# Kernel tuning notes

Hardware: AMD Instinct MI355X
Metric: run time of the kernel (lower is better)

## Reference

```python
import jax, jax.numpy as jnp
import numpy as np

B, G, N = 32, 512, 512          # batch, group (POMO rollouts), problem size
EMB, H, DK = 128, 8, 16          # embedding_dim, head_num, qkv_dim (H*DK == EMB)
E, FH, K = 8, 512, 2             # num_experts, ff_hidden_dim, top-k
SQRT_EMB = 11.313708498984761    # sqrt(128), model_params['sqrt_embedding_dim']
CLIP = 10.0                      # logit_clipping


def setup_inputs() -> dict:
    key = jax.random.key(0)
    ks = jax.random.split(key, 22)
    s = 0.05
    d = {}
    d["pref"] = jax.random.uniform(ks[0], (2,), dtype=jnp.float32)
    d["graph"] = jax.random.normal(ks[1], (B, 1, EMB), dtype=jnp.float32)
    d["capacity"] = jax.random.uniform(ks[2], (B, G), dtype=jnp.float32)
    d["encoded_nodes"] = jax.random.normal(ks[3], (B, N, EMB), dtype=jnp.float32)
    d["ninf_mask"] = jnp.zeros((B, G, N), dtype=jnp.float32)
    # hyper-network MLP (note: original has NO activations between hyper_fc layers)
    d["fc1_w"] = jax.random.normal(ks[4], (256, 2)) * s
    d["fc1_b"] = jax.random.normal(ks[5], (256,)) * s
    d["fc2_w"] = jax.random.normal(ks[6], (256, 256)) * s
    d["fc2_b"] = jax.random.normal(ks[7], (256,)) * s
    d["fc3_w"] = jax.random.normal(ks[8], (8, 256)) * s
    d["fc3_b"] = jax.random.normal(ks[9], (8,)) * s
    # hyper heads producing the attention weight matrices (Linear(embd_dim=2, out), no bias)
    d["hWq"] = jax.random.normal(ks[10], ((1 + EMB) * H * DK, 2)) * 0.02
    d["hWk"] = jax.random.normal(ks[11], (EMB * H * DK, 2)) * 0.02
    d["hWv"] = jax.random.normal(ks[12], (EMB * H * DK, 2)) * 0.02
    d["hWc"] = jax.random.normal(ks[13], (EMB * H * DK, 2)) * 0.02
    # MoE combine layer: gating (token input + 8-dim pref embedding) and E expert MLPs
    d["gate_w"] = jax.random.normal(ks[14], (H * DK, E)) * s
    d["gate_pref_w"] = jax.random.normal(ks[15], (8, E)) * s
    d["e_w1"] = jax.random.normal(ks[16], (E, FH, H * DK)) * (1.0 / np.sqrt(H * DK))
    d["e_b1"] = jnp.zeros((E, FH), dtype=jnp.float32)
    d["e_w2"] = jax.random.normal(ks[17], (E, EMB, FH)) * (1.0 / np.sqrt(FH))
    d["e_b2"] = jnp.zeros((E, EMB), dtype=jnp.float32)
    d = {k2: v.astype(jnp.float32) for k2, v in d.items()}
    return d


def _heads(x):  # [B, n, H*DK] -> [B, H, n, DK]
    b, n, _ = x.shape
    return x.reshape(b, n, H, DK).transpose(0, 2, 1, 3)


def reference(pref, graph, capacity, encoded_nodes, ninf_mask,
              fc1_w, fc1_b, fc2_w, fc2_b, fc3_w, fc3_b,
              hWq, hWk, hWv, hWc,
              gate_w, gate_pref_w, e_w1, e_b1, e_w2, e_b2):
    # ---- assign(pref): hypernet generates attention weight matrices ----
    h = fc1_w @ pref + fc1_b
    h = fc2_w @ h + fc2_b
    mid = fc3_w @ h + fc3_b                      # [8] == mid_embd_pref
    Wq = (hWq @ mid[0:2]).reshape(H * DK, 1 + EMB)
    Wk = (hWk @ mid[2:4]).reshape(H * DK, EMB)
    Wv = (hWv @ mid[4:6]).reshape(H * DK, EMB)
    Wc = (hWc @ mid[6:8]).reshape(H * DK, EMB)
    # ---- set_kv ----
    k = _heads(encoded_nodes @ Wk.T)             # [B,H,N,DK]
    v = _heads(encoded_nodes @ Wv.T)
    # ---- forward ----
    inp = jnp.concatenate(
        [jnp.broadcast_to(graph, (B, G, EMB)), capacity[:, :, None]], axis=2)
    q = _heads(inp @ Wq.T)                       # [B,H,G,DK]
    score = jnp.einsum('bhgd,bhnd->bhgn', q, k) / jnp.sqrt(jnp.float32(DK))
    score = score + ninf_mask[:, None, :, :]
    attn = jax.nn.softmax(score, axis=3)
    out = jnp.einsum('bhgn,bhnd->bhgd', attn, v)
    out = out.transpose(0, 2, 1, 3).reshape(B, G, H * DK)   # [B,G,128]
    # ---- MoE combine (noisy top-k gating, deterministic at inference) ----
    logits = out @ gate_w + mid @ gate_pref_w    # [B,G,E]
    vals, idx = jax.lax.top_k(logits, K)
    gv = jax.nn.softmax(vals, axis=-1)           # softmax over selected k (T=1)
    gates = jnp.sum(jax.nn.one_hot(idx, E, dtype=out.dtype) * gv[..., None], axis=-2)
    hdn = jax.nn.relu(jnp.einsum('bgi,ehi->bgeh', out, e_w1) + e_b1)
    y = jnp.einsum('bgeh,eoh->bgeo', hdn, e_w2) + e_b2
    moe_out = jnp.einsum('bgeo,bge->bgo', y, gates)          # [B,G,EMB]
    # ---- combine + tanh-clipped masked softmax over nodes ----
    mh = moe_out @ Wc.T                           # [B,G,EMB]
    sc = jnp.einsum('bge,bne->bgn', mh, encoded_nodes) / SQRT_EMB
    probs = jax.nn.softmax(CLIP * jnp.tanh(sc) + ninf_mask, axis=2)
    return probs
```

## Files before the change

kernel.cpp:

```cpp
#include <hip/hip_runtime.h>


typedef __attribute__((ext_vector_type(8))) __bf16 bf16x8;
typedef __attribute__((ext_vector_type(4))) float f32x4;

static constexpr long OFF_MID   = 0;
static constexpr long OFF_PREFL = 8;
static constexpr long OFF_WL    = 16;
static constexpr long OFF_WKB   = 256;
static constexpr long OFF_WVB   = 8448;
static constexpr long OFF_WCB   = 16640;
static constexpr long OFF_QB    = 24832;
static constexpr long OFF_MFLAG = 28928;
static constexpr long OFF_CNT   = 33024;
static constexpr long OFF_TOK   = 33032;
static constexpr long OFF_WGT   = 164104;
static constexpr long OFF_AO    = 295176;
static constexpr long OFF_MH    = 2392328;
static constexpr long OFF_ENCB  = 3440904;

__device__ __forceinline__ unsigned f2bf(float x) {
  union { float f; unsigned u; } v; v.f = x;
  return ((v.u + 0x7FFFu + ((v.u >> 16) & 1u)) >> 16) & 0xFFFFu;
}
__device__ __forceinline__ float bflo(unsigned u) {
  union { unsigned u; float f; } v; v.u = u << 16; return v.f;
}
__device__ __forceinline__ float bfhi(unsigned u) {
  union { unsigned u; float f; } v; v.u = u & 0xFFFF0000u; return v.f;
}

__global__ __launch_bounds__(256)
void k_prep1(const float* __restrict__ pref, const float* __restrict__ fc1w,
             const float* __restrict__ fc1b, const float* __restrict__ fc2w,
             const float* __restrict__ fc2b, const float* __restrict__ fc3w,
             const float* __restrict__ fc3b, const float* __restrict__ gpw,
             const float* __restrict__ hWq, const float* __restrict__ mask,
             const float* __restrict__ ew1, const float* __restrict__ ew2,
             const float* __restrict__ enc,
             unsigned short* __restrict__ w1b, unsigned short* __restrict__ w2b,
             unsigned short* __restrict__ encb, float* __restrict__ ws) {
  const int bid = blockIdx.x;
  const int tid = threadIdx.x;
  if (bid == 0) {
    __shared__ float h1[256];
    __shared__ float h2[256];
    __shared__ float mid[8];
    const float p0 = pref[0], p1 = pref[1];
    h1[tid] = fc1w[2*tid]*p0 + fc1w[2*tid+1]*p1 + fc1b[tid];
    __syncthreads();
    float s = 0.f;
    for (int j = 0; j < 256; ++j) s = fmaf(fc2w[tid*256+j], h1[j], s);
    h2[tid] = s + fc2b[tid];
    __syncthreads();
    if (tid < 8) {
      float s2 = 0.f;
      for (int j = 0; j < 256; ++j) s2 = fmaf(fc3w[tid*256+j], h2[j], s2);
      mid[tid] = s2 + fc3b[tid];
    }
    __syncthreads();
    if (tid < 8) {
      ws[OFF_MID + tid] = mid[tid];
      float s3 = 0.f;
      for (int i = 0; i < 8; ++i) s3 = fmaf(mid[i], gpw[i*8 + tid], s3);
      ws[OFF_PREFL + tid] = s3;
      ((int*)(ws + OFF_CNT))[tid] = 0;
    }
    if (tid >= 16 && tid < 144) {
      const int o = tid - 16;
      ws[OFF_WL + o] = hWq[((long)o*129 + 128)*2]*mid[0]
                     + hWq[((long)o*129 + 128)*2 + 1]*mid[1];
    }
    return;
  }
  if (bid <= 3072) {
    const int i = (bid-1)*256 + tid;
    const float* src;
    unsigned short* dst;
    if (i < 131072)      { src = ew1 + (long)i*4;          dst = w1b + (long)i*4; }
    else if (i < 262144) { src = ew2 + (long)(i-131072)*4; dst = w2b + (long)(i-131072)*4; }
    else                 { src = enc + (long)(i-262144)*4; dst = encb + (long)(i-262144)*4; }
    const float4 v = *(const float4*)src;
    uint2 p;
    p.x = f2bf(v.x) | (f2bf(v.y) << 16);
    p.y = f2bf(v.z) | (f2bf(v.w) << 16);
    *(uint2*)dst = p;
    return;
  }
  __shared__ int fl[8];
  const int rowbase = (bid - 3073) * 8;
  const int r = tid >> 5, seg = tid & 31;
  if (tid < 8) fl[tid] = 0;
  __syncthreads();
  const float* mrow = mask + (long)(rowbase + r)*512 + seg*16;
  int nz = 0;
#pragma unroll
  for (int c = 0; c < 4; ++c) {
    const float4 v = *(const float4*)(mrow + c*4);
    nz |= (v.x != 0.f) | (v.y != 0.f) | (v.z != 0.f) | (v.w != 0.f);
  }
  if (nz) atomicOr(&fl[r], 1);
  __syncthreads();
  if (tid < 8) ((char*)(ws + OFF_MFLAG))[rowbase + tid] = (char)fl[tid];
}

__global__ __launch_bounds__(256)
void k_prep2(const float* __restrict__ graph,
             const float* __restrict__ hWq, const float* __restrict__ hWk,
             const float* __restrict__ hWv, const float* __restrict__ hWc,
             float* __restrict__ ws) {
  const int bid = blockIdx.x;
  const int tid = threadIdx.x;
  __shared__ float mid[8];
  __shared__ float g[2][128];
  if (tid < 8) mid[tid] = ws[OFF_MID + tid];
  __syncthreads();
  if (bid < 192) {
    const int i = bid*256 + tid;
    if (i < 16384) {
      ((unsigned short*)(ws + OFF_WKB))[i] =
          (unsigned short)f2bf(hWk[2*i]*mid[2] + hWk[2*i+1]*mid[3]);
    } else if (i < 32768) {
      const int j = i - 16384;
      ((unsigned short*)(ws + OFF_WVB))[j] =
          (unsigned short)f2bf(hWv[2*j]*mid[4] + hWv[2*j+1]*mid[5]);
    } else {
      const int j = i - 32768;
      ((unsigned short*)(ws + OFF_WCB))[j] =
          (unsigned short)f2bf(hWc[2*j]*mid[6] + hWc[2*j+1]*mid[7]);
    }
    return;
  }
  const int qb = bid - 192;
  const int b0 = qb*2;
  {
    const int bb = tid >> 7, ii = tid & 127;
    g[bb][ii] = graph[(b0+bb)*128 + ii];
  }
  __syncthreads();
  const float m0 = mid[0], m1 = mid[1];
  const int bb = tid >> 7, o = tid & 127;
  const float* hq = hWq + (long)o*129*2;
  float acc = 0.f;
  for (int i2 = 0; i2 < 128; ++i2) {
    const float w = hq[2*i2]*m0 + hq[2*i2+1]*m1;
    acc = fmaf(g[bb][i2], w, acc);
  }
  ws[OFF_QB + (b0+bb)*128 + o] = acc;
}

__device__ __forceinline__ bf16x8 ld_frag(const unsigned short* base, int row, int bytecol) {
  const int addr = row*256 + (bytecol ^ ((row & 7) << 4));
  return *(const bf16x8*)((const char*)base + addr);
}

__global__ __launch_bounds__(256)
void k_kv(const unsigned short* __restrict__ encb,
          const unsigned short* __restrict__ wkb,
          const unsigned short* __restrict__ wvb,
          unsigned short* __restrict__ Kb, unsigned short* __restrict__ Vtg) {
  __shared__ unsigned short Ws[128*128];
  __shared__ unsigned short Xs[64*128];
  const int tid = threadIdx.x;
  const int nbase = blockIdx.x * 64;
  const unsigned short* Wb = blockIdx.y ? wvb : wkb;
#pragma unroll
  for (int s = 0; s < 8; ++s) {
    const int id = tid + s*256;
    const int fr = id >> 4, c16 = id & 15;
    const uint4 v = *(const uint4*)(Wb + (long)fr*128 + c16*8);
    *(uint4*)((char*)Ws + fr*256 + ((c16*16) ^ ((fr & 7) << 4))) = v;
  }
#pragma unroll
  for (int s = 0; s < 4; ++s) {
    const int id = tid + s*256;
    const int r = id >> 4, c16 = id & 15;
    const uint4 v = *(const uint4*)(encb + (long)(nbase + r)*128 + c16*8);
    *(uint4*)((char*)Xs + r*256 + ((c16*16) ^ ((r & 7) << 4))) = v;
  }
  __syncthreads();
  const int w = tid >> 6, l = tid & 63, lq = l >> 4, lr = l & 15;
  f32x4 acc[2][4];
#pragma unroll
  for (int a = 0; a < 2; ++a)
#pragma unroll
    for (int m = 0; m < 4; ++m) acc[a][m] = (f32x4){0.f, 0.f, 0.f, 0.f};
#pragma unroll
  for (int ks = 0; ks < 4; ++ks) {
    const int bcol = ks*64 + lq*16;
    const bf16x8 a0 = ld_frag(Ws, (2*w  )*16 + lr, bcol);
    const bf16x8 a1 = ld_frag(Ws, (2*w+1)*16 + lr, bcol);
    const bf16x8 b0 = ld_frag(Xs, 0*16 + lr, bcol);
    const bf16x8 b1 = ld_frag(Xs, 1*16 + lr, bcol);
    const bf16x8 b2 = ld_frag(Xs, 2*16 + lr, bcol);
    const bf16x8 b3 = ld_frag(Xs, 3*16 + lr, bcol);
    acc[0][0] = __builtin_amdgcn_mfma_f32_16x16x32_bf16(a0, b0, acc[0][0], 0, 0, 0);
    acc[0][1] = __builtin_amdgcn_mfma_f32_16x16x32_bf16(a0, b1, acc[0][1], 0, 0, 0);
    acc[0][2] = __builtin_amdgcn_mfma_f32_16x16x32_bf16(a0, b2, acc[0][2], 0, 0, 0);
    acc[0][3] = __builtin_amdgcn_mfma_f32_16x16x32_bf16(a0, b3, acc[0][3], 0, 0, 0);
    acc[1][0] = __builtin_amdgcn_mfma_f32_16x16x32_bf16(a1, b0, acc[1][0], 0, 0, 0);
    acc[1][1] = __builtin_amdgcn_mfma_f32_16x16x32_bf16(a1, b1, acc[1][1], 0, 0, 0);
    acc[1][2] = __builtin_amdgcn_mfma_f32_16x16x32_bf16(a1, b2, acc[1][2], 0, 0, 0);
    acc[1][3] = __builtin_amdgcn_mfma_f32_16x16x32_bf16(a1, b3, acc[1][3], 0, 0, 0);
  }
  if (blockIdx.y == 0) {
#pragma unroll
    for (int obi = 0; obi < 2; ++obi) {
      const int o0 = (2*w + obi)*16 + lq*4;
#pragma unroll
      for (int mb = 0; mb < 4; ++mb) {
        const long n = nbase + mb*16 + lr;
        uint2 pp;
        pp.x = f2bf(acc[obi][mb][0]) | (f2bf(acc[obi][mb][1]) << 16);
        pp.y = f2bf(acc[obi][mb][2]) | (f2bf(acc[obi][mb][3]) << 16);
        *(uint2*)(Kb + n*128 + o0) = pp;
      }
    }
  } else {
    const int b = nbase >> 9;
    const int nn0 = nbase & 511;
#pragma unroll
    for (int obi = 0; obi < 2; ++obi) {
      const int o0 = (2*w + obi)*16 + lq*4;
#pragma unroll
      for (int mb = 0; mb < 4; ++mb) {
        const int nn = nn0 + mb*16 + lr;
#pragma unroll
        for (int j = 0; j < 4; ++j) {
          const int o = o0 + j;
          Vtg[(((long)b*8 + (o >> 4))*16 + (o & 15))*512 + nn] =
              (unsigned short)f2bf(acc[obi][mb][j]);
        }
      }
    }
  }
}

__global__ __launch_bounds__(256)
void k_mh(const float* __restrict__ Y0, const float* __restrict__ Y1,
          const unsigned short* __restrict__ wcb,
          unsigned short* __restrict__ mhb) {
  __shared__ unsigned short Ws[128*128];
  __shared__ unsigned short Xs[64*128];
  const int tid = threadIdx.x;
  const int nbase = blockIdx.x * 64;
#pragma unroll
  for (int s = 0; s < 8; ++s) {
    const int id = tid + s*256;
    const int fr = id >> 4, c16 = id & 15;
    const uint4 v = *(const uint4*)(wcb + (long)fr*128 + c16*8);
    *(uint4*)((char*)Ws + fr*256 + ((c16*16) ^ ((fr & 7) << 4))) = v;
  }
#pragma unroll
  for (int s = 0; s < 4; ++s) {
    const int id = tid + s*256;
    const int r = id >> 4, c16 = id & 15;
    const long base = (long)(nbase + r)*128 + c16*8;
    const float4 a0 = *(const float4*)(Y0 + base);
    const float4 a1 = *(const float4*)(Y0 + base + 4);
    const float4 b0 = *(const float4*)(Y1 + base);
    const float4 b1 = *(const float4*)(Y1 + base + 4);
    uint4 p;
    p.x = f2bf(a0.x + b0.x) | (f2bf(a0.y + b0.y) << 16);
    p.y = f2bf(a0.z + b0.z) | (f2bf(a0.w + b0.w) << 16);
    p.z = f2bf(a1.x + b1.x) | (f2bf(a1.y + b1.y) << 16);
    p.w = f2bf(a1.z + b1.z) | (f2bf(a1.w + b1.w) << 16);
    *(uint4*)((char*)Xs + r*256 + ((c16*16) ^ ((r & 7) << 4))) = p;
  }
  __syncthreads();
  const int w = tid >> 6, l = tid & 63, lq = l >> 4, lr = l & 15;
  f32x4 acc[2][4];
#pragma unroll
  for (int a = 0; a < 2; ++a)
#pragma unroll
    for (int m = 0; m < 4; ++m) acc[a][m] = (f32x4){0.f, 0.f, 0.f, 0.f};
#pragma unroll
  for (int ks = 0; ks < 4; ++ks) {
    const int bcol = ks*64 + lq*16;
    const bf16x8 a0 = ld_frag(Ws, (2*w  )*16 + lr, bcol);
    const bf16x8 a1 = ld_frag(Ws, (2*w+1)*16 + lr, bcol);
    const bf16x8 b0 = ld_frag(Xs, 0*16 + lr, bcol);
    const bf16x8 b1 = ld_frag(Xs, 1*16 + lr, bcol);
    const bf16x8 b2 = ld_frag(Xs, 2*16 + lr, bcol);
    const bf16x8 b3 = ld_frag(Xs, 3*16 + lr, bcol);
    acc[0][0] = __builtin_amdgcn_mfma_f32_16x16x32_bf16(a0, b0, acc[0][0], 0, 0, 0);
    acc[0][1] = __builtin_amdgcn_mfma_f32_16x16x32_bf16(a0, b1, acc[0][1], 0, 0, 0);
    acc[0][2] = __builtin_amdgcn_mfma_f32_16x16x32_bf16(a0, b2, acc[0][2], 0, 0, 0);
    acc[0][3] = __builtin_amdgcn_mfma_f32_16x16x32_bf16(a0, b3, acc[0][3], 0, 0, 0);
    acc[1][0] = __builtin_amdgcn_mfma_f32_16x16x32_bf16(a1, b0, acc[1][0], 0, 0, 0);
    acc[1][1] = __builtin_amdgcn_mfma_f32_16x16x32_bf16(a1, b1, acc[1][1], 0, 0, 0);
    acc[1][2] = __builtin_amdgcn_mfma_f32_16x16x32_bf16(a1, b2, acc[1][2], 0, 0, 0);
    acc[1][3] = __builtin_amdgcn_mfma_f32_16x16x32_bf16(a1, b3, acc[1][3], 0, 0, 0);
  }
#pragma unroll
  for (int obi = 0; obi < 2; ++obi) {
    const int o0 = (2*w + obi)*16 + lq*4;
#pragma unroll
    for (int mb = 0; mb < 4; ++mb) {
      const long n = nbase + mb*16 + lr;
      uint2 pp;
      pp.x = f2bf(acc[obi][mb][0]) | (f2bf(acc[obi][mb][1]) << 16);
      pp.y = f2bf(acc[obi][mb][2]) | (f2bf(acc[obi][mb][3]) << 16);
      *(uint2*)(mhb + n*128 + o0) = pp;
    }
  }
}

__global__ __launch_bounds__(512, 8)
void k_attn(const unsigned short* __restrict__ Kb,
            const unsigned short* __restrict__ Vtg,
            const float* __restrict__ ws, const float* __restrict__ cap,
            const float* __restrict__ mask, unsigned short* __restrict__ AOb) {
  const int bid = blockIdx.x;
  const int b = bid & 31, h = (bid >> 5) & 7, qh = bid >> 8;
  __shared__ unsigned short Kbf[512*24];
  __shared__ unsigned short Vt[16*536];
  __shared__ unsigned short Ps[8*16*40];
  const int tid = threadIdx.x;
#pragma unroll
  for (int it = 0; it < 2; ++it) {
    const int i = tid + it*512;
    const int n = i >> 1, hf = i & 1;
    const uint4 kv = *(const uint4*)(Kb + (long)(b*512 + n)*128 + h*16 + hf*8);
    *(uint4*)(Kbf + n*24 + hf*8) = kv;
    const int d = i >> 6, c = i & 63;
    const uint4 vv = *(const uint4*)(Vtg + ((long)(b*8 + h)*16 + d)*512 + c*8);
    *(uint4*)(Vt + d*536 + c*8) = vv;
  }
  const int w = tid >> 6, l = tid & 63;
  const int lq = l >> 4, lr = l & 15;
  const int grow = qh*128 + w*16 + lr;
  bf16x8 qf;
  {
    union { uint4 u; bf16x8 v; } cv;
    cv.u = make_uint4(0u, 0u, 0u, 0u);
    if (lq < 2) {
      const float* qbp = ws + OFF_QB + b*128 + h*16 + lq*8;
      const float* wlp = ws + OFF_WL + h*16 + lq*8;
      const float cp = cap[b*512 + grow];
      float qv[8];
#pragma unroll
      for (int j = 0; j < 8; ++j) qv[j] = (qbp[j] + cp*wlp[j]) * 0.25f;
      cv.u.x = f2bf(qv[0]) | (f2bf(qv[1]) << 16);
      cv.u.y = f2bf(qv[2]) | (f2bf(qv[3]) << 16);
      cv.u.z = f2bf(qv[4]) | (f2bf(qv[5]) << 16);
      cv.u.w = f2bf(qv[6]) | (f2bf(qv[7]) << 16);
    }
    qf = cv.v;
  }
  const int mf = ((const char*)(ws + OFF_MFLAG))[b*512 + grow];
  const bool usemask = __any(mf != 0);
  unsigned short* Pw = Ps + w*16*40;
  const int psw = (lr & 3) << 3;
  __syncthreads();
  float lsum = 0.f;
  f32x4 oacc = {0.f, 0.f, 0.f, 0.f};
  const float* mrow = mask + ((long)(b*512 + grow))*512 + lq*4;
  for (int qc = 0; qc < 16; ++qc) {
    const int n0 = qc*32;
    f32x4 s[2];
#pragma unroll
    for (int nb = 0; nb < 2; ++nb) {
      bf16x8 kf;
      {
        union { uint4 u; bf16x8 v; } cv;
        cv.u = make_uint4(0u, 0u, 0u, 0u);
        if (lq < 2) cv.u = *(const uint4*)(Kbf + (n0 + nb*16 + lr)*24 + lq*8);
        kf = cv.v;
      }
      s[nb] = __builtin_amdgcn_mfma_f32_16x16x32_bf16(
          kf, qf, (f32x4){0.f, 0.f, 0.f, 0.f}, 0, 0, 0);
      if (usemask) {
        const float4 mk = *(const float4*)(mrow + n0 + nb*16);
        s[nb][0] += mk.x; s[nb][1] += mk.y; s[nb][2] += mk.z; s[nb][3] += mk.w;
      }
    }
#pragma unroll
    for (int nb = 0; nb < 2; ++nb) {
      const float e0 = __expf(s[nb][0]);
      const float e1 = __expf(s[nb][1]);
      const float e2 = __expf(s[nb][2]);
      const float e3 = __expf(s[nb][3]);
      lsum += (e0 + e1) + (e2 + e3);
      uint2 pp;
      asm("v_cvt_pk_bf16_f32 %0, %1, %2" : "=v"(pp.x) : "v"(e0), "v"(e1));
      asm("v_cvt_pk_bf16_f32 %0, %1, %2" : "=v"(pp.y) : "v"(e2), "v"(e3));
      *(uint2*)(Pw + lr*40 + ((nb*16 + lq*4) ^ psw)) = pp;
    }
    const bf16x8 va = *(const bf16x8*)(Vt + lr*536 + n0 + lq*8);
    const bf16x8 pb = *(const bf16x8*)(Pw + lr*40 + (lq*8 ^ psw));
    oacc = __builtin_amdgcn_mfma_f32_16x16x32_bf16(va, pb, oacc, 0, 0, 0);
  }
  lsum += __shfl_xor(lsum, 16);
  lsum += __shfl_xor(lsum, 32);
  const float inv = 1.f / lsum;
  uint2 op;
  op.x = f2bf(oacc[0]*inv) | (f2bf(oacc[1]*inv) << 16);
  op.y = f2bf(oacc[2]*inv) | (f2bf(oacc[3]*inv) << 16);
  *(uint2*)(AOb + (long)(b*512 + grow)*128 + h*16 + lq*4) = op;
}

__global__ __launch_bounds__(256)
void k_gate(const unsigned short* __restrict__ AOb, const float* __restrict__ gw,
            float* __restrict__ ws) {
  const int tid = threadIdx.x;
  const int t = blockIdx.x*256 + tid;
  const unsigned short* x = AOb + (long)t*128;
  float lg[8];
  {
    const float* pl = ws + OFF_PREFL;
#pragma unroll
    for (int e = 0; e < 8; ++e) lg[e] = pl[e];
  }
  for (int i = 0; i < 128; i += 8) {
    const uint4 xv = *(const uint4*)(x + i);
    float xf[8];
    xf[0] = bflo(xv.x); xf[1] = bfhi(xv.x);
    xf[2] = bflo(xv.y); xf[3] = bfhi(xv.y);
    xf[4] = bflo(xv.z); xf[5] = bfhi(xv.z);
    xf[6] = bflo(xv.w); xf[7] = bfhi(xv.w);
#pragma unroll
    for (int u = 0; u < 8; ++u) {
      const float xi = xf[u];
      const float4 ga = *(const float4*)(gw + (i+u)*8);
      const float4 gb = *(const float4*)(gw + (i+u)*8 + 4);
      lg[0] = fmaf(xi, ga.x, lg[0]); lg[1] = fmaf(xi, ga.y, lg[1]);
      lg[2] = fmaf(xi, ga.z, lg[2]); lg[3] = fmaf(xi, ga.w, lg[3]);
      lg[4] = fmaf(xi, gb.x, lg[4]); lg[5] = fmaf(xi, gb.y, lg[5]);
      lg[6] = fmaf(xi, gb.z, lg[6]); lg[7] = fmaf(xi, gb.w, lg[7]);
    }
  }
  int i0 = 0; float v0 = lg[0];
#pragma unroll
  for (int e = 1; e < 8; ++e) if (lg[e] > v0) { v0 = lg[e]; i0 = e; }
  int i1 = -1; float v1 = -1e30f;
#pragma unroll
  for (int e = 0; e < 8; ++e) if (e != i0 && lg[e] > v1) { v1 = lg[e]; i1 = e; }
  const float e1 = __expf(v1 - v0);
  const float w0 = 1.f / (1.f + e1);
  const float w1 = 1.f - w0;
  __shared__ int bcnt[8];
  __shared__ int gbase[8];
  if (tid < 8) bcnt[tid] = 0;
  __syncthreads();
  const int p0 = atomicAdd(&bcnt[i0], 1);
  const int p1 = atomicAdd(&bcnt[i1], 1);
  __syncthreads();
  if (tid < 8) {
    int* cnt = (int*)(ws + OFF_CNT);
    gbase[tid] = (bcnt[tid] > 0) ? atomicAdd(&cnt[tid], bcnt[tid]) : 0;
  }
  __syncthreads();
  int* tokp = (int*)(ws + OFF_TOK);
  float* wgtp = ws + OFF_WGT;
  const int s0 = gbase[i0] + p0;
  tokp[i0*16384 + s0] = t;
  wgtp[i0*16384 + s0] = w0;
  const int s1 = gbase[i1] + p1;
  tokp[i1*16384 + s1] = t | (1 << 30);
  wgtp[i1*16384 + s1] = w1;
}

__global__ __launch_bounds__(256)
void k_moe(const unsigned short* __restrict__ AOb,
           const unsigned short* __restrict__ w1b,
           const unsigned short* __restrict__ w2b,
           const float* __restrict__ eb1, const float* __restrict__ eb2,
           float* __restrict__ ws,
           float* __restrict__ Y0, float* __restrict__ Y1) {
  const int e = blockIdx.y;
  const int ce = ((const int*)(ws + OFF_CNT))[e];
  const int base = blockIdx.x * 64;
  if (base >= ce) return;
  const int nt = min(64, ce - base);

  __shared__ unsigned short Xs[64*128];
  __shared__ unsigned short Wts[128*128];
  __shared__ unsigned short Hs[64*128];
  __shared__ float seb1[512];
  __shared__ float seb2[128];
  __shared__ int   stok[64];
  __shared__ float swgt[64];

  const int tid = threadIdx.x;
  if (tid < 64) {
    if (tid < nt) {
      stok[tid] = ((const int*)(ws + OFF_TOK))[e*16384 + base + tid];
      swgt[tid] = (ws + OFF_WGT)[e*16384 + base + tid];
    } else { stok[tid] = -1; swgt[tid] = 0.f; }
  }
  for (int i = tid; i < 512; i += 256) seb1[i] = eb1[e*512 + i];
  if (tid < 128) seb2[tid] = eb2[e*128 + tid];
  __syncthreads();

#pragma unroll
  for (int r4 = 0; r4 < 4; ++r4) {
    const int id = tid + r4*256;
    const int r = id >> 4, c16 = id & 15;
    const int pk = stok[r];
    uint4 v = make_uint4(0u, 0u, 0u, 0u);
    if (pk >= 0) v = *(const uint4*)(AOb + (long)(pk & 0x3FFFFFFF)*128 + c16*8);
    *(uint4*)((char*)Xs + r*256 + ((c16*16) ^ ((r & 7) << 4))) = v;
  }

  const int w  = tid >> 6;
  const int l  = tid & 63;
  const int lq = l >> 4;
  const int lr = l & 15;

  f32x4 yacc[2][4];
#pragma unroll
  for (int a = 0; a < 2; ++a)
#pragma unroll
    for (int m = 0; m < 4; ++m) yacc[a][m] = (f32x4){0.f, 0.f, 0.f, 0.f};

  for (int fc = 0; fc < 4; ++fc) {
    __syncthreads();
    {
      const long wb = (long)(e*512 + fc*128) * 128;
#pragma unroll
      for (int s = 0; s < 8; ++s) {
        const int id = tid + s*256;
        const int fr = id >> 4, c16 = id & 15;
        const uint4 v = *(const uint4*)(w1b + wb + (long)fr*128 + c16*8);
        *(uint4*)((char*)Wts + fr*256 + ((c16*16) ^ ((fr & 7) << 4))) = v;
      }
    }
    __syncthreads();
    f32x4 hacc[2][4];
#pragma unroll
    for (int a = 0; a < 2; ++a)
#pragma unroll
      for (int m = 0; m < 4; ++m) hacc[a][m] = (f32x4){0.f, 0.f, 0.f, 0.f};
#pragma unroll
    for (int ks = 0; ks < 4; ++ks) {
      const int bcol = ks*64 + lq*16;
      const bf16x8 a0 = ld_frag(Wts, (2*w  )*16 + lr, bcol);
      const bf16x8 a1 = ld_frag(Wts, (2*w+1)*16 + lr, bcol);
      const bf16x8 b0 = ld_frag(Xs,  0*16 + lr, bcol);
      const bf16x8 b1 = ld_frag(Xs,  1*16 + lr, bcol);
      const bf16x8 b2 = ld_frag(Xs,  2*16 + lr, bcol);
      const bf16x8 b3 = ld_frag(Xs,  3*16 + lr, bcol);
      hacc[0][0] = __builtin_amdgcn_mfma_f32_16x16x32_bf16(a0, b0, hacc[0][0], 0, 0, 0);
      hacc[0][1] = __builtin_amdgcn_mfma_f32_16x16x32_bf16(a0, b1, hacc[0][1], 0, 0, 0);
      hacc[0][2] = __builtin_amdgcn_mfma_f32_16x16x32_bf16(a0, b2, hacc[0][2], 0, 0, 0);
      hacc[0][3] = __builtin_amdgcn_mfma_f32_16x16x32_bf16(a0, b3, hacc[0][3], 0, 0, 0);
      hacc[1][0] = __builtin_amdgcn_mfma_f32_16x16x32_bf16(a1, b0, hacc[1][0], 0, 0, 0);
      hacc[1][1] = __builtin_amdgcn_mfma_f32_16x16x32_bf16(a1, b1, hacc[1][1], 0, 0, 0);
      hacc[1][2] = __builtin_amdgcn_mfma_f32_16x16x32_bf16(a1, b2, hacc[1][2], 0, 0, 0);
      hacc[1][3] = __builtin_amdgcn_mfma_f32_16x16x32_bf16(a1, b3, hacc[1][3], 0, 0, 0);
    }
    __syncthreads();
#pragma unroll
    for (int fbi = 0; fbi < 2; ++fbi) {
      const int fb = (2*w + fbi)*16 + lq*4;
      const float4 bia = *(const float4*)&seb1[fc*128 + fb];
#pragma unroll
      for (int mb = 0; mb < 4; ++mb) {
        const int m = mb*16 + lr;
        const float h0 = fmaxf(hacc[fbi][mb][0] + bia.x, 0.f);
        const float h1 = fmaxf(hacc[fbi][mb][1] + bia.y, 0.f);
        const float h2 = fmaxf(hacc[fbi][mb][2] + bia.z, 0.f);
        const float h3 = fmaxf(hacc[fbi][mb][3] + bia.w, 0.f);
        uint2 p;
        p.x = f2bf(h0) | (f2bf(h1) << 16);
        p.y = f2bf(h2) | (f2bf(h3) << 16);
        const int bc = (fb*2) ^ ((m & 7) << 4);
        *(uint2*)((char*)Hs + m*256 + bc) = p;
      }
    }
    {
      const long wb = (long)(e*128) * 512 + fc*128;
#pragma unroll
      for (int s = 0; s < 8; ++s) {
        const int id = tid + s*256;
        const int orr = id >> 4, c16 = id & 15;
        const uint4 v = *(const uint4*)(w2b + wb + (long)orr*512 + c16*8);
        *(uint4*)((char*)Wts + orr*256 + ((c16*16) ^ ((orr & 7) << 4))) = v;
      }
    }
    __syncthreads();
#pragma unroll
    for (int ks = 0; ks < 4; ++ks) {
      const int bcol = ks*64 + lq*16;
      const bf16x8 a0 = ld_frag(Wts, (2*w  )*16 + lr, bcol);
      const bf16x8 a1 = ld_frag(Wts, (2*w+1)*16 + lr, bcol);
      const bf16x8 b0 = ld_frag(Hs,  0*16 + lr, bcol);
      const bf16x8 b1 = ld_frag(Hs,  1*16 + lr, bcol);
      const bf16x8 b2 = ld_frag(Hs,  2*16 + lr, bcol);
      const bf16x8 b3 = ld_frag(Hs,  3*16 + lr, bcol);
      yacc[0][0] = __builtin_amdgcn_mfma_f32_16x16x32_bf16(a0, b0, yacc[0][0], 0, 0, 0);
      yacc[0][1] = __builtin_amdgcn_mfma_f32_16x16x32_bf16(a0, b1, yacc[0][1], 0, 0, 0);
      yacc[0][2] = __builtin_amdgcn_mfma_f32_16x16x32_bf16(a0, b2, yacc[0][2], 0, 0, 0);
      yacc[0][3] = __builtin_amdgcn_mfma_f32_16x16x32_bf16(a0, b3, yacc[0][3], 0, 0, 0);
      yacc[1][0] = __builtin_amdgcn_mfma_f32_16x16x32_bf16(a1, b0, yacc[1][0], 0, 0, 0);
      yacc[1][1] = __builtin_amdgcn_mfma_f32_16x16x32_bf16(a1, b1, yacc[1][1], 0, 0, 0);
      yacc[1][2] = __builtin_amdgcn_mfma_f32_16x16x32_bf16(a1, b2, yacc[1][2], 0, 0, 0);
      yacc[1][3] = __builtin_amdgcn_mfma_f32_16x16x32_bf16(a1, b3, yacc[1][3], 0, 0, 0);
    }
  }
#pragma unroll
  for (int obi = 0; obi < 2; ++obi) {
    const int ob = (2*w + obi)*16 + lq*4;
    const float4 b2 = *(const float4*)&seb2[ob];
#pragma unroll
    for (int mb = 0; mb < 4; ++mb) {
      const int tl = mb*16 + lr;
      if (tl < nt) {
        const int pk = stok[tl];
        const int tk = pk & 0x3FFFFFFF;
        const float wgt = swgt[tl];
        float* Yp = ((pk >> 30) ? Y1 : Y0) + (long)tk*128 + ob;
        float4 o;
        o.x = (yacc[obi][mb][0] + b2.x) * wgt;
        o.y = (yacc[obi][mb][1] + b2.y) * wgt;
        o.z = (yacc[obi][mb][2] + b2.z) * wgt;
        o.w = (yacc[obi][mb][3] + b2.w) * wgt;
        *(float4*)Yp = o;
      }
    }
  }
}

__global__ __launch_bounds__(512)
void k_gemm2f(const unsigned short* __restrict__ mhb,
              const unsigned short* __restrict__ encb,
              const float* __restrict__ mask,
              const char* __restrict__ mflag,
              float* __restrict__ out) {
  const int bid = blockIdx.x;
  const int b = bid & 31, rt = bid >> 5;
  __shared__ unsigned short Amh[64*128];
  __shared__ unsigned short Bch[512*32];
  __shared__ float red[64][9];
  __shared__ char sfl[64];
  const int tid = threadIdx.x;
  const int w = tid >> 6, l = tid & 63, lq = l >> 4, lr = l & 15;
  const long rowbase = (long)b*512 + rt*64;
#pragma unroll
  for (int s = 0; s < 2; ++s) {
    const int id = tid + s*512;
    const int r = id >> 4, c16 = id & 15;
    const uint4 v = *(const uint4*)(mhb + (rowbase + r)*128 + c16*8);
    *(uint4*)((char*)Amh + r*256 + ((c16*16) ^ ((r & 7) << 4))) = v;
  }
  if (tid < 64) sfl[tid] = mflag[rowbase + tid];
  f32x4 acc[4][4];
#pragma unroll
  for (int mi = 0; mi < 4; ++mi)
#pragma unroll
    for (int ni = 0; ni < 4; ++ni) acc[mi][ni] = (f32x4){0.f, 0.f, 0.f, 0.f};
  for (int kc = 0; kc < 4; ++kc) {
    __syncthreads();
#pragma unroll
    for (int s = 0; s < 4; ++s) {
      const int id = tid + s*512;
      const int n = id >> 2, sl = id & 3;
      const uint4 v = *(const uint4*)(encb + ((long)b*512 + n)*128 + kc*32 + sl*8);
      *(uint4*)((char*)Bch + n*64 + ((sl*16) ^ ((n & 3) << 4))) = v;
    }
    __syncthreads();
    bf16x8 af[4], bfr[4];
#pragma unroll
    for (int mi = 0; mi < 4; ++mi) {
      const int r = mi*16 + lr;
      af[mi] = *(const bf16x8*)((const char*)Amh + r*256 + ((kc*64 + lq*16) ^ ((r & 7) << 4)));
    }
#pragma unroll
    for (int ni = 0; ni < 4; ++ni) {
      const int n = w*64 + ni*16 + lr;
      bfr[ni] = *(const bf16x8*)((const char*)Bch + n*64 + ((lq*16) ^ ((n & 3) << 4)));
    }
#pragma unroll
    for (int mi = 0; mi < 4; ++mi)
#pragma unroll
      for (int ni = 0; ni < 4; ++ni)
        acc[mi][ni] = __builtin_amdgcn_mfma_f32_16x16x32_bf16(af[mi], bfr[ni], acc[mi][ni], 0, 0, 0);
  }
  const float ISC = 1.f/11.313708498984761f;
  float rsum[4][4];
#pragma unroll
  for (int mi = 0; mi < 4; ++mi)
#pragma unroll
    for (int j = 0; j < 4; ++j) rsum[mi][j] = 0.f;
#pragma unroll
  for (int mi = 0; mi < 4; ++mi) {
#pragma unroll
    for (int j = 0; j < 4; ++j) {
      const int rl = mi*16 + lq*4 + j;
      const bool um = sfl[rl] != 0;
      const float* mrow = mask + (rowbase + rl)*512 + w*64 + lr;
#pragma unroll
      for (int ni = 0; ni < 4; ++ni) {
        const float sc = acc[mi][ni][j] * ISC;
        const float mv = um ? mrow[ni*16] : 0.f;
        const float li = 10.f*tanhf(sc) + mv;
        const float e = __expf(li - 10.f);
        acc[mi][ni][j] = e;
        rsum[mi][j] += e;
      }
    }
  }
#pragma unroll
  for (int mi = 0; mi < 4; ++mi)
#pragma unroll
    for (int j = 0; j < 4; ++j) {
#pragma unroll
      for (int o = 1; o < 16; o <<= 1) rsum[mi][j] += __shfl_xor(rsum[mi][j], o);
    }
  if (lr == 0) {
#pragma unroll
    for (int mi = 0; mi < 4; ++mi)
#pragma unroll
      for (int j = 0; j < 4; ++j) red[mi*16 + lq*4 + j][w] = rsum[mi][j];
  }
  __syncthreads();
  if (tid < 64) {
    float s = 0.f;
#pragma unroll
    for (int wv = 0; wv < 8; ++wv) s += red[tid][wv];
    red[tid][8] = 1.f / s;
  }
  __syncthreads();
#pragma unroll
  for (int mi = 0; mi < 4; ++mi) {
#pragma unroll
    for (int j = 0; j < 4; ++j) {
      const int rl = mi*16 + lq*4 + j;
      const float inv = red[rl][8];
      float* orow = out + (rowbase + rl)*512 + w*64 + lr;
#pragma unroll
      for (int ni = 0; ni < 4; ++ni) orow[ni*16] = acc[mi][ni][j] * inv;
    }
  }
}

extern "C" void kernel_launch(void* const* d_in, const int* in_sizes, int n_in,
                              void* d_out, int out_size, void* d_ws, size_t ws_size,
                              hipStream_t stream) {
  (void)in_sizes; (void)n_in; (void)out_size; (void)ws_size;
  const float* pref  = (const float*)d_in[0];
  const float* graph = (const float*)d_in[1];
  const float* cap   = (const float*)d_in[2];
  const float* enc   = (const float*)d_in[3];
  const float* mask  = (const float*)d_in[4];
  const float* fc1w  = (const float*)d_in[5];
  const float* fc1b  = (const float*)d_in[6];
  const float* fc2w  = (const float*)d_in[7];
  const float* fc2b  = (const float*)d_in[8];
  const float* fc3w  = (const float*)d_in[9];
  const float* fc3b  = (const float*)d_in[10];
  const float* hWq   = (const float*)d_in[11];
  const float* hWk   = (const float*)d_in[12];
  const float* hWv   = (const float*)d_in[13];
  const float* hWc   = (const float*)d_in[14];
  const float* gw    = (const float*)d_in[15];
  const float* gpw   = (const float*)d_in[16];
  const float* ew1   = (const float*)d_in[17];
  const float* eb1   = (const float*)d_in[18];
  const float* ew2   = (const float*)d_in[19];
  const float* eb2   = (const float*)d_in[20];
  float* ws  = (float*)d_ws;
  float* out = (float*)d_out;
  unsigned short* Kbuf = (unsigned short*)out;
  unsigned short* Vtg  = (unsigned short*)(out + 1048576);
  float* Y0 = out;
  float* Y1 = out + 2097152;
  unsigned short* ew1b = (unsigned short*)(out + 4194304);
  unsigned short* ew2b = (unsigned short*)(out + 4456448);
  unsigned short* AOb  = (unsigned short*)(ws + OFF_AO);
  unsigned short* mhb  = (unsigned short*)(ws + OFF_MH);
  unsigned short* encb = (unsigned short*)(ws + OFF_ENCB);
  unsigned short* wkb  = (unsigned short*)(ws + OFF_WKB);
  unsigned short* wvb  = (unsigned short*)(ws + OFF_WVB);
  unsigned short* wcb  = (unsigned short*)(ws + OFF_WCB);
  const char* mflag = (const char*)(ws + OFF_MFLAG);

  k_prep1<<<5121, 256, 0, stream>>>(pref, fc1w, fc1b, fc2w, fc2b, fc3w, fc3b,
                                    gpw, hWq, mask, ew1, ew2, enc,
                                    ew1b, ew2b, encb, ws);
  k_prep2<<<208, 256, 0, stream>>>(graph, hWq, hWk, hWv, hWc, ws);
  k_kv<<<dim3(256, 2), 256, 0, stream>>>(encb, wkb, wvb, Kbuf, Vtg);
  k_attn<<<1024, 512, 0, stream>>>(Kbuf, Vtg, ws, cap, mask, AOb);
  k_gate<<<64, 256, 0, stream>>>(AOb, gw, ws);
  k_moe<<<dim3(256, 8), 256, 0, stream>>>(AOb, ew1b, ew2b, eb1, eb2, ws, Y0, Y1);
  k_mh<<<256, 256, 0, stream>>>(Y0, Y1, wcb, mhb);
  k_gemm2f<<<256, 512, 0, stream>>>(mhb, encb, mask, mflag, out);
}
```

Baseline: 119.4 us.

## Fuse Wc projection into final GEMM, store MoE outputs in bf16, split attn accumulators

Removes the k_mh kernel: the final logits kernel now loads both MoE output halves, sums them, multiplies by Wc in shared memory with MFMA, and reuses the result as the A operand for the node-score GEMM. This saves one launch and the round trip of the mh buffer. MoE outputs are now written as bf16 instead of fp32, which halves that traffic but adds one extra rounding before the sum. The attention PV loop is unrolled by two and uses two alternating accumulators to break the MFMA dependency chain.

Result: faster. 112.4 us (-5.8%).

```diff
diff --git a/kernel.cpp b/kernel.cpp
--- a/kernel.cpp
+++ b/kernel.cpp
@@ -16,7 +16,8 @@
 static constexpr long OFF_TOK   = 33032;
 static constexpr long OFF_WGT   = 164104;
 static constexpr long OFF_AO    = 295176;
-static constexpr long OFF_MH    = 2392328;
+static constexpr long OFF_Y0    = 1343752;
+static constexpr long OFF_Y1    = 2392328;
 static constexpr long OFF_ENCB  = 3440904;
 
 __device__ __forceinline__ unsigned f2bf(float x) {
@@ -236,76 +237,6 @@
   }
 }
 
-__global__ __launch_bounds__(256)
-void k_mh(const float* __restrict__ Y0, const float* __restrict__ Y1,
-          const unsigned short* __restrict__ wcb,
-          unsigned short* __restrict__ mhb) {
-  __shared__ unsigned short Ws[128*128];
-  __shared__ unsigned short Xs[64*128];
-  const int tid = threadIdx.x;
-  const int nbase = blockIdx.x * 64;
-#pragma unroll
-  for (int s = 0; s < 8; ++s) {
-    const int id = tid + s*256;
-    const int fr = id >> 4, c16 = id & 15;
-    const uint4 v = *(const uint4*)(wcb + (long)fr*128 + c16*8);
-    *(uint4*)((char*)Ws + fr*256 + ((c16*16) ^ ((fr & 7) << 4))) = v;
-  }
-#pragma unroll
-  for (int s = 0; s < 4; ++s) {
-    const int id = tid + s*256;
-    const int r = id >> 4, c16 = id & 15;
-    const long base = (long)(nbase + r)*128 + c16*8;
-    const float4 a0 = *(const float4*)(Y0 + base);
-    const float4 a1 = *(const float4*)(Y0 + base + 4);
-    const float4 b0 = *(const float4*)(Y1 + base);
-    const float4 b1 = *(const float4*)(Y1 + base + 4);
-    uint4 p;
-    p.x = f2bf(a0.x + b0.x) | (f2bf(a0.y + b0.y) << 16);
-    p.y = f2bf(a0.z + b0.z) | (f2bf(a0.w + b0.w) << 16);
-    p.z = f2bf(a1.x + b1.x) | (f2bf(a1.y + b1.y) << 16);
-    p.w = f2bf(a1.z + b1.z) | (f2bf(a1.w + b1.w) << 16);
-    *(uint4*)((char*)Xs + r*256 + ((c16*16) ^ ((r & 7) << 4))) = p;
-  }
-  __syncthreads();
-  const int w = tid >> 6, l = tid & 63, lq = l >> 4, lr = l & 15;
-  f32x4 acc[2][4];
-#pragma unroll
-  for (int a = 0; a < 2; ++a)
-#pragma unroll
-    for (int m = 0; m < 4; ++m) acc[a][m] = (f32x4){0.f, 0.f, 0.f, 0.f};
-#pragma unroll
-  for (int ks = 0; ks < 4; ++ks) {
-    const int bcol = ks*64 + lq*16;
-    const bf16x8 a0 = ld_frag(Ws, (2*w  )*16 + lr, bcol);
-    const bf16x8 a1 = ld_frag(Ws, (2*w+1)*16 + lr, bcol);
-    const bf16x8 b0 = ld_frag(Xs, 0*16 + lr, bcol);
-    const bf16x8 b1 = ld_frag(Xs, 1*16 + lr, bcol);
-    const bf16x8 b2 = ld_frag(Xs, 2*16 + lr, bcol);
-    const bf16x8 b3 = ld_frag(Xs, 3*16 + lr, bcol);
-    acc[0][0] = __builtin_amdgcn_mfma_f32_16x16x32_bf16(a0, b0, acc[0][0], 0, 0, 0);
-    acc[0][1] = __builtin_amdgcn_mfma_f32_16x16x32_bf16(a0, b1, acc[0][1], 0, 0, 0);
-    acc[0][2] = __builtin_amdgcn_mfma_f32_16x16x32_bf16(a0, b2, acc[0][2], 0, 0, 0);
-    acc[0][3] = __builtin_amdgcn_mfma_f32_16x16x32_bf16(a0, b3, acc[0][3], 0, 0, 0);
-    acc[1][0] = __builtin_amdgcn_mfma_f32_16x16x32_bf16(a1, b0, acc[1][0], 0, 0, 0);
-    acc[1][1] = __builtin_amdgcn_mfma_f32_16x16x32_bf16(a1, b1, acc[1][1], 0, 0, 0);
-    acc[1][2] = __builtin_amdgcn_mfma_f32_16x16x32_bf16(a1, b2, acc[1][2], 0, 0, 0);
-    acc[1][3] = __builtin_amdgcn_mfma_f32_16x16x32_bf16(a1, b3, acc[1][3], 0, 0, 0);
-  }
-#pragma unroll
-  for (int obi = 0; obi < 2; ++obi) {
-    const int o0 = (2*w + obi)*16 + lq*4;
-#pragma unroll
-    for (int mb = 0; mb < 4; ++mb) {
-      const long n = nbase + mb*16 + lr;
-      uint2 pp;
-      pp.x = f2bf(acc[obi][mb][0]) | (f2bf(acc[obi][mb][1]) << 16);
-      pp.y = f2bf(acc[obi][mb][2]) | (f2bf(acc[obi][mb][3]) << 16);
-      *(uint2*)(mhb + n*128 + o0) = pp;
-    }
-  }
-}
-
 __global__ __launch_bounds__(512, 8)
 void k_attn(const unsigned short* __restrict__ Kb,
             const unsigned short* __restrict__ Vtg,
@@ -354,8 +285,10 @@
   const int psw = (lr & 3) << 3;
   __syncthreads();
   float lsum = 0.f;
-  f32x4 oacc = {0.f, 0.f, 0.f, 0.f};
+  f32x4 oaccA = {0.f, 0.f, 0.f, 0.f};
+  f32x4 oaccB = {0.f, 0.f, 0.f, 0.f};
   const float* mrow = mask + ((long)(b*512 + grow))*512 + lq*4;
+#pragma unroll 2
   for (int qc = 0; qc < 16; ++qc) {
     const int n0 = qc*32;
     f32x4 s[2];
@@ -389,14 +322,15 @@
     }
     const bf16x8 va = *(const bf16x8*)(Vt + lr*536 + n0 + lq*8);
     const bf16x8 pb = *(const bf16x8*)(Pw + lr*40 + (lq*8 ^ psw));
-    oacc = __builtin_amdgcn_mfma_f32_16x16x32_bf16(va, pb, oacc, 0, 0, 0);
+    if (qc & 1) oaccB = __builtin_amdgcn_mfma_f32_16x16x32_bf16(va, pb, oaccB, 0, 0, 0);
+    else        oaccA = __builtin_amdgcn_mfma_f32_16x16x32_bf16(va, pb, oaccA, 0, 0, 0);
   }
   lsum += __shfl_xor(lsum, 16);
   lsum += __shfl_xor(lsum, 32);
   const float inv = 1.f / lsum;
   uint2 op;
-  op.x = f2bf(oacc[0]*inv) | (f2bf(oacc[1]*inv) << 16);
-  op.y = f2bf(oacc[2]*inv) | (f2bf(oacc[3]*inv) << 16);
+  op.x = f2bf((oaccA[0]+oaccB[0])*inv) | (f2bf((oaccA[1]+oaccB[1])*inv) << 16);
+  op.y = f2bf((oaccA[2]+oaccB[2])*inv) | (f2bf((oaccA[3]+oaccB[3])*inv) << 16);
   *(uint2*)(AOb + (long)(b*512 + grow)*128 + h*16 + lq*4) = op;
 }
 
@@ -467,7 +401,7 @@
            const unsigned short* __restrict__ w2b,
            const float* __restrict__ eb1, const float* __restrict__ eb2,
            float* __restrict__ ws,
-           float* __restrict__ Y0, float* __restrict__ Y1) {
+           unsigned short* __restrict__ Y0b, unsigned short* __restrict__ Y1b) {
   const int e = blockIdx.y;
   const int ce = ((const int*)(ws + OFF_CNT))[e];
   const int base = blockIdx.x * 64;
@@ -610,20 +544,22 @@
         const int pk = stok[tl];
         const int tk = pk & 0x3FFFFFFF;
         const float wgt = swgt[tl];
-        float* Yp = ((pk >> 30) ? Y1 : Y0) + (long)tk*128 + ob;
-        float4 o;
-        o.x = (yacc[obi][mb][0] + b2.x) * wgt;
-        o.y = (yacc[obi][mb][1] + b2.y) * wgt;
-        o.z = (yacc[obi][mb][2] + b2.z) * wgt;
-        o.w = (yacc[obi][mb][3] + b2.w) * wgt;
-        *(float4*)Yp = o;
+        unsigned short* Yp = ((pk >> 30) ? Y1b : Y0b) + (long)tk*128 + ob;
+        uint2 p;
+        p.x = f2bf((yacc[obi][mb][0] + b2.x) * wgt)
+            | (f2bf((yacc[obi][mb][1] + b2.y) * wgt) << 16);
+        p.y = f2bf((yacc[obi][mb][2] + b2.z) * wgt)
+            | (f2bf((yacc[obi][mb][3] + b2.w) * wgt) << 16);
+        *(uint2*)Yp = p;
       }
     }
   }
 }
 
 __global__ __launch_bounds__(512)
-void k_gemm2f(const unsigned short* __restrict__ mhb,
+void k_gemm2f(const unsigned short* __restrict__ Y0b,
+              const unsigned short* __restrict__ Y1b,
+              const unsigned short* __restrict__ wcb,
               const unsigned short* __restrict__ encb,
               const float* __restrict__ mask,
               const char* __restrict__ mflag,
@@ -641,10 +577,53 @@
   for (int s = 0; s < 2; ++s) {
     const int id = tid + s*512;
     const int r = id >> 4, c16 = id & 15;
-    const uint4 v = *(const uint4*)(mhb + (rowbase + r)*128 + c16*8);
-    *(uint4*)((char*)Amh + r*256 + ((c16*16) ^ ((r & 7) << 4))) = v;
+    const long yb = (rowbase + r)*128 + c16*8;
+    const uint4 a = *(const uint4*)(Y0b + yb);
+    const uint4 c = *(const uint4*)(Y1b + yb);
+    uint4 p;
+    p.x = f2bf(bflo(a.x)+bflo(c.x)) | (f2bf(bfhi(a.x)+bfhi(c.x)) << 16);
+    p.y = f2bf(bflo(a.y)+bflo(c.y)) | (f2bf(bfhi(a.y)+bfhi(c.y)) << 16);
+    p.z = f2bf(bflo(a.z)+bflo(c.z)) | (f2bf(bfhi(a.z)+bfhi(c.z)) << 16);
+    p.w = f2bf(bflo(a.w)+bflo(c.w)) | (f2bf(bfhi(a.w)+bfhi(c.w)) << 16);
+    *(uint4*)((char*)Amh + r*256 + ((c16*16) ^ ((r & 7) << 4))) = p;
+  }
+#pragma unroll
+  for (int s = 0; s < 4; ++s) {
+    const int id = tid + s*512;
+    const int fr = id >> 4, c16 = id & 15;
+    const uint4 v = *(const uint4*)(wcb + (long)fr*128 + c16*8);
+    *(uint4*)((char*)Bch + fr*256 + ((c16*16) ^ ((fr & 7) << 4))) = v;
   }
   if (tid < 64) sfl[tid] = mflag[rowbase + tid];
+  __syncthreads();
+  {
+    f32x4 macc[4];
+#pragma unroll
+    for (int m = 0; m < 4; ++m) macc[m] = (f32x4){0.f, 0.f, 0.f, 0.f};
+#pragma unroll
+    for (int ks = 0; ks < 4; ++ks) {
+      const int bcol = ks*64 + lq*16;
+      const bf16x8 a0 = ld_frag(Bch, w*16 + lr, bcol);
+      const bf16x8 b0 = ld_frag(Amh, 0*16 + lr, bcol);
+      const bf16x8 b1 = ld_frag(Amh, 1*16 + lr, bcol);
+      const bf16x8 b2 = ld_frag(Amh, 2*16 + lr, bcol);
+      const bf16x8 b3 = ld_frag(Amh, 3*16 + lr, bcol);
+      macc[0] = __builtin_amdgcn_mfma_f32_16x16x32_bf16(a0, b0, macc[0], 0, 0, 0);
+      macc[1] = __builtin_amdgcn_mfma_f32_16x16x32_bf16(a0, b1, macc[1], 0, 0, 0);
+      macc[2] = __builtin_amdgcn_mfma_f32_16x16x32_bf16(a0, b2, macc[2], 0, 0, 0);
+      macc[3] = __builtin_amdgcn_mfma_f32_16x16x32_bf16(a0, b3, macc[3], 0, 0, 0);
+    }
+    __syncthreads();
+    const int o0 = w*16 + lq*4;
+#pragma unroll
+    for (int mb = 0; mb < 4; ++mb) {
+      const int m = mb*16 + lr;
+      uint2 p;
+      p.x = f2bf(macc[mb][0]) | (f2bf(macc[mb][1]) << 16);
+      p.y = f2bf(macc[mb][2]) | (f2bf(macc[mb][3]) << 16);
+      *(uint2*)((char*)Amh + m*256 + ((o0*2) ^ ((m & 7) << 4))) = p;
+    }
+  }
   f32x4 acc[4][4];
 #pragma unroll
   for (int mi = 0; mi < 4; ++mi)
@@ -764,12 +743,11 @@
   float* out = (float*)d_out;
   unsigned short* Kbuf = (unsigned short*)out;
   unsigned short* Vtg  = (unsigned short*)(out + 1048576);
-  float* Y0 = out;
-  float* Y1 = out + 2097152;
   unsigned short* ew1b = (unsigned short*)(out + 4194304);
   unsigned short* ew2b = (unsigned short*)(out + 4456448);
   unsigned short* AOb  = (unsigned short*)(ws + OFF_AO);
-  unsigned short* mhb  = (unsigned short*)(ws + OFF_MH);
+  unsigned short* Y0b  = (unsigned short*)(ws + OFF_Y0);
+  unsigned short* Y1b  = (unsigned short*)(ws + OFF_Y1);
   unsigned short* encb = (unsigned short*)(ws + OFF_ENCB);
   unsigned short* wkb  = (unsigned short*)(ws + OFF_WKB);
   unsigned short* wvb  = (unsigned short*)(ws + OFF_WVB);
@@ -783,7 +761,6 @@
   k_kv<<<dim3(256, 2), 256, 0, stream>>>(encb, wkb, wvb, Kbuf, Vtg);
   k_attn<<<1024, 512, 0, stream>>>(Kbuf, Vtg, ws, cap, mask, AOb);
   k_gate<<<64, 256, 0, stream>>>(AOb, gw, ws);
-  k_moe<<<dim3(256, 8), 256, 0, stream>>>(AOb, ew1b, ew2b, eb1, eb2, ws, Y0, Y1);
-  k_mh<<<256, 256, 0, stream>>>(Y0, Y1, wcb, mhb);
-  k_gemm2f<<<256, 512, 0, stream>>>(mhb, encb, mask, mflag, out);
-}
+  k_moe<<<dim3(256, 8), 256, 0, stream>>>(AOb, ew1b, ew2b, eb1, eb2, ws, Y0b, Y1b);
+  k_gemm2f<<<256, 512, 0, stream>>>(Y0b, Y1b, wcb, encb, mask, mflag, out);
+}
```
